# Performance work log

Measured on AMD Instinct MI355X. Metric: run time of the kernel, lower is better.

Reference implementation:

```python
import math
import jax, jax.numpy as jnp
import numpy as np

N, E = 40000, 640000
IN, OUT, T, R, H = 128, 128, 8, 16, 8
DK = OUT // H


def _tproj(x, W, types):
    # x: (N, I), W: (T, I, O), types: (N,) -> per-node type-indexed projection (N, O)
    allp = jnp.einsum('ni,tio->nto', x, W)  # T is tiny (8), cheap vs gathering per-node W
    return jnp.take_along_axis(allp, types[:, None, None], axis=1)[:, 0]


def setup_inputs() -> dict:
    key = jax.random.key(0)
    ks = jax.random.split(key, 12)
    h = jax.random.normal(ks[0], (N, IN), jnp.float32)
    src = jax.random.randint(ks[1], (E,), 0, N)
    dst = jax.random.randint(ks[2], (E,), 0, N)
    ntype = jax.random.randint(ks[3], (N,), 0, T)
    etype = jax.random.randint(ks[4], (E,), 0, R)
    s = 0.05  # scale torch.rand-style U(0,1) params for stable softmax numerics
    k_weight = jax.random.uniform(ks[5], (T, IN, OUT), jnp.float32) * s
    q_weight = jax.random.uniform(ks[6], (T, IN, OUT), jnp.float32) * s
    v_weight = jax.random.uniform(ks[7], (T, IN, OUT), jnp.float32) * s
    a_weight = jax.random.uniform(ks[8], (T, OUT, OUT), jnp.float32) * s
    relation_att = jax.random.uniform(ks[9], (R, H, DK, DK), jnp.float32) * s
    relation_msg = jax.random.uniform(ks[10], (R, H, DK, DK), jnp.float32) * s
    relation_pri = jnp.ones((R, H), jnp.float32)
    skip = jnp.ones((T, H), jnp.float32)
    return dict(h=h, k_weight=k_weight, q_weight=q_weight, v_weight=v_weight,
                a_weight=a_weight, relation_pri=relation_pri, relation_att=relation_att,
                relation_msg=relation_msg, skip=skip, src=src, dst=dst,
                ntype=ntype, etype=etype)


def reference(h, k_weight, q_weight, v_weight, a_weight, relation_pri,
              relation_att, relation_msg, skip, src, dst, ntype, etype):
    n, _ = h.shape
    nT, _, out = k_weight.shape
    nR, nH, dk, _ = relation_att.shape
    e = src.shape[0]
    sqrt_dk = math.sqrt(out)  # matches self.sqrt_dk = sqrt(out_feat_dim)

    # per-node type-specific k/v/q projections (equivalent to per-edge gathered bmm)
    k_n = _tproj(h, k_weight, ntype)
    v_n = _tproj(h, v_weight, ntype)
    q_n = _tproj(h, q_weight, ntype)

    k = k_n[src].reshape(e, nH, dk)
    v = v_n[src].reshape(e, nH, dk)
    q = q_n[dst].reshape(e, nH, dk)

    # relation-specific transforms; loop over small fixed relation set to avoid
    # materializing the (E, H, dk, dk) gathered weight tensor
    k2 = jnp.zeros_like(k)
    v2 = jnp.zeros_like(v)
    for r in range(nR):
        m = (etype == r)[:, None, None]
        k2 = k2 + jnp.where(m, jnp.einsum('ehd,hdc->ehc', k, relation_att[r]), 0.0)
        v2 = v2 + jnp.where(m, jnp.einsum('ehd,hdc->ehc', v, relation_msg[r]), 0.0)

    # attention score per edge/head
    attn = jnp.einsum('ehd,ehd->eh', k2, q) * relation_pri[etype] / sqrt_dk

    # segment (edge) softmax over destination nodes
    amax = jax.lax.stop_gradient(jax.ops.segment_max(attn, dst, num_segments=n))
    p = jnp.exp(attn - amax[dst])
    denom = jax.ops.segment_sum(p, dst, num_segments=n)
    alpha = p / denom[dst]  # (E, H)

    # weighted message scatter-sum -> mailbox reduce
    msg = alpha[:, :, None] * v2  # (E, H, dk)
    t = jax.ops.segment_sum(msg.reshape(e, nH * dk), dst, num_segments=n)  # (N, OUT)

    # node update: type-indexed output transform, per-head sigmoid skip gate
    trans = _tproj(t, a_weight, ntype)  # (N, OUT)
    gate = jax.nn.sigmoid(skip[ntype])  # (N, H)
    out_h = (trans.reshape(n, nH, dk) * gate[:, :, None]).reshape(n, out)
    return out_h


if __name__ == '__main__':
    inp = setup_inputs()
    o = reference(**inp)
    print(o.shape, o.dtype)
```

## Files before the change

### kernel.cpp

```cpp
#include <hip/hip_runtime.h>
#include <hip/hip_fp16.h>
#include <type_traits>

#define NN 40000
#define EE 640000
#define TT 8
#define RR 16
#define HH 8
#define DIM 128
#define NEG_BIG (-3.402823466e38f)
#define INV_SQRT_OUT 0.08838834764831845f


__global__ void zero_k(int* __restrict__ p, int n) {
  int i = blockIdx.x * blockDim.x + threadIdx.x;
  if (i < n) p[i] = 0;
}


__global__ void hist_nodes_k(const int* __restrict__ ntype, int* __restrict__ cnt_t) {
  __shared__ int lc[TT];
  int tid = threadIdx.x;
  if (tid < TT) lc[tid] = 0;
  __syncthreads();
  int n = blockIdx.x * blockDim.x + tid;
  if (n < NN) atomicAdd(&lc[ntype[n]], 1);
  __syncthreads();
  if (tid < TT && lc[tid]) atomicAdd(&cnt_t[tid], lc[tid]);
}

__global__ void hist_edges_k(const int* __restrict__ dst, const int* __restrict__ etype,
                             int* __restrict__ deg, int* __restrict__ cnt_r) {
  __shared__ int lc[RR];
  int tid = threadIdx.x;
  if (tid < RR) lc[tid] = 0;
  __syncthreads();
  int e = blockIdx.x * blockDim.x + tid;
  if (e < EE) {
    atomicAdd(&deg[dst[e]], 1);
    atomicAdd(&lc[etype[e]], 1);
  }
  __syncthreads();
  if (tid < RR && lc[tid]) atomicAdd(&cnt_r[tid], lc[tid]);
}

__global__ __launch_bounds__(1024) void scan_k(
    const int* __restrict__ cnt_t, int* __restrict__ toff, int* __restrict__ tcur,
    const int* __restrict__ cnt_r, int* __restrict__ roff, int* __restrict__ rcur,
    const int* __restrict__ deg, int* __restrict__ off, int* __restrict__ cur) {
  __shared__ int tot[1024];
  int tid = threadIdx.x;
  if (tid == 0) {
    int a = 0;
    for (int t = 0; t < TT; ++t) { toff[t] = a; tcur[t] = a; a += cnt_t[t]; }
    toff[TT] = a;
    a = 0;
    for (int r = 0; r < RR; ++r) { roff[r] = a; rcur[r] = a; a += cnt_r[r]; }
    roff[RR] = a;
  }
  const int NPT = (NN + 1023) / 1024;
  int base = tid * NPT;
  int s = 0;
  for (int k = 0; k < NPT; ++k) { int i = base + k; if (i < NN) s += deg[i]; }
  tot[tid] = s;
  __syncthreads();
  for (int st = 1; st < 1024; st <<= 1) {
    int v = (tid >= st) ? tot[tid - st] : 0;
    __syncthreads();
    tot[tid] += v;
    __syncthreads();
  }
  int run = (tid > 0) ? tot[tid - 1] : 0;
  for (int k = 0; k < NPT; ++k) {
    int i = base + k;
    if (i < NN) {
      cur[i] = run;
      run += deg[i];
      off[i + 1] = run;
    }
  }
  if (tid == 0) off[0] = 0;
}

__global__ void scatter_nodes_k(const int* __restrict__ ntype, int* __restrict__ tcur,
                                int* __restrict__ perm) {
  __shared__ int lc[TT], lb[TT];
  int tid = threadIdx.x;
  if (tid < TT) lc[tid] = 0;
  __syncthreads();
  int n = blockIdx.x * blockDim.x + tid;
  int t = 0, rank = 0;
  bool valid = (n < NN);
  if (valid) { t = ntype[n]; rank = atomicAdd(&lc[t], 1); }
  __syncthreads();
  if (tid < TT && lc[tid]) lb[tid] = atomicAdd(&tcur[tid], lc[tid]);
  __syncthreads();
  if (valid) perm[lb[t] + rank] = n;
}

__global__ void scatter_edges_k(const int* __restrict__ dst, const int* __restrict__ etype,
                                int* __restrict__ cur, int* __restrict__ rcur,
                                int* __restrict__ eid_dst, int* __restrict__ eid_r) {
  __shared__ int lc[RR], lb[RR];
  int tid = threadIdx.x;
  if (tid < RR) lc[tid] = 0;
  __syncthreads();
  int e = blockIdx.x * blockDim.x + tid;
  int r = 0, rank = 0;
  bool valid = (e < EE);
  if (valid) {
    int dd = dst[e];
    int p = atomicAdd(&cur[dd], 1);
    eid_dst[p] = e;
    r = etype[e];
    rank = atomicAdd(&lc[r], 1);
  }
  __syncthreads();
  if (tid < RR && lc[tid]) lb[tid] = atomicAdd(&rcur[tid], lc[tid]);
  __syncthreads();
  if (valid) eid_r[lb[r] + rank] = e;
}


template <int NMAT, bool GATE>
__global__ __launch_bounds__(256) void proj_k(
    const float* __restrict__ X,
    const float* __restrict__ W0, const float* __restrict__ W1, const float* __restrict__ W2,
    float* O0, float* O1, float* O2,
    const int* __restrict__ perm, const int* __restrict__ toff,
    const float* __restrict__ skipw) {
  __shared__ float xs[64 * DIM];
  __shared__ int pid[64];
  int t = blockIdx.y;
  int b0 = toff[t] + blockIdx.x * 64;
  int bn = toff[t + 1] - b0;
  if (bn <= 0) return;
  if (bn > 64) bn = 64;
  int tid = threadIdx.x;
  if (tid < 64) pid[tid] = perm[b0 + ((tid < bn) ? tid : 0)];
  __syncthreads();
  for (int s = tid; s < 64 * 32; s += 256) {
    int row = s >> 5, c4 = s & 31;
    *(float4*)&xs[row * DIM + c4 * 4] = *(const float4*)&X[(size_t)pid[row] * DIM + c4 * 4];
  }
  __syncthreads();
  int p = tid & 63, q = tid >> 6;
  int oc = 2 * p;
  float gate = 1.f;
  if (GATE) {
    float sk = skipw[t * HH + (oc >> 4)];
    gate = 1.f / (1.f + __expf(-sk));
  }
  const float* Ws[3] = {W0, W1, W2};
  float* Os[3] = {O0, O1, O2};
#pragma unroll
  for (int mat = 0; mat < NMAT; ++mat) {
    const float* W = Ws[mat] + (size_t)t * DIM * DIM;
    float acc0[16], acc1[16];
#pragma unroll
    for (int m = 0; m < 16; ++m) { acc0[m] = 0.f; acc1[m] = 0.f; }
    for (int i4 = 0; i4 < 32; ++i4) {
      int i = i4 * 4;
      float2 w0 = *(const float2*)&W[(i + 0) * DIM + oc];
      float2 w1 = *(const float2*)&W[(i + 1) * DIM + oc];
      float2 w2 = *(const float2*)&W[(i + 2) * DIM + oc];
      float2 w3 = *(const float2*)&W[(i + 3) * DIM + oc];
#pragma unroll
      for (int m = 0; m < 16; ++m) {
        float4 xv = *(const float4*)&xs[(q * 16 + m) * DIM + i];
        acc0[m] += xv.x * w0.x + xv.y * w1.x + xv.z * w2.x + xv.w * w3.x;
        acc1[m] += xv.x * w0.y + xv.y * w1.y + xv.z * w2.y + xv.w * w3.y;
      }
    }
    float* O = Os[mat];
#pragma unroll
    for (int m = 0; m < 16; ++m) {
      float2 val = {acc0[m] * gate, acc1[m] * gate};
      *(float2*)&O[(size_t)pid[q * 16 + m] * DIM + oc] = val;
    }
  }
}


template <typename VT, bool WV2>
__global__ __launch_bounds__(256) void edge_k(
    const float* __restrict__ kn, const float* __restrict__ qn, const float* __restrict__ vn,
    const float* __restrict__ attw, const float* __restrict__ msgw, const float* __restrict__ pri,
    const int* __restrict__ src, const int* __restrict__ dst,
    const int* __restrict__ roff, const int* __restrict__ eidr,
    float* __restrict__ attn_ws, VT* __restrict__ v2) {
  int r = blockIdx.y;
  int base = roff[r];
  int cnt = roff[r + 1] - base;
  int tile0 = blockIdx.x * 256;
  if (tile0 >= cnt) return;
  __shared__ float att_sw[2048];
  __shared__ float msg_sw[2048];
  __shared__ int eid[256];
  int tid = threadIdx.x;
  {
    const float* A = attw + (size_t)r * 2048;
    const float* M = msgw + (size_t)r * 2048;
    for (int idx = tid; idx < 2048; idx += 256) {
      int hh = idx >> 8, dd = (idx >> 4) & 15, cc = idx & 15;
      int u = ((((hh << 6) + (cc << 2) + (dd >> 2)) ^ hh) << 2) + (dd & 3);
      att_sw[u] = A[idx];
      if (WV2) msg_sw[u] = M[idx];
    }
  }
  eid[tid] = (tile0 + tid < cnt) ? eidr[base + tile0 + tid] : -1;
  __syncthreads();
  int h = tid & 7;
  float prih = pri[r * HH + h] * INV_SQRT_OUT;
  for (int pass = 0; pass < 8; ++pass) {
    int e = eid[(pass << 5) + (tid >> 3)];
    if (e < 0) continue;
    int s = src[e], d = dst[e];
    float kk[16], qq[16];
    const float* kp = kn + (size_t)s * DIM + h * 16;
    *(float4*)&kk[0] = *(const float4*)(kp + 0);
    *(float4*)&kk[4] = *(const float4*)(kp + 4);
    *(float4*)&kk[8] = *(const float4*)(kp + 8);
    *(float4*)&kk[12] = *(const float4*)(kp + 12);
    const float* qp = qn + (size_t)d * DIM + h * 16;
    *(float4*)&qq[0] = *(const float4*)(qp + 0);
    *(float4*)&qq[4] = *(const float4*)(qp + 4);
    *(float4*)&qq[8] = *(const float4*)(qp + 8);
    *(float4*)&qq[12] = *(const float4*)(qp + 12);
    float attn = 0.f;
#pragma unroll
    for (int c = 0; c < 16; ++c) {
      float k2c = 0.f;
#pragma unroll
      for (int dq = 0; dq < 4; ++dq) {
        float4 av = *(const float4*)&att_sw[((((h << 6) + (c << 2) + dq) ^ h) << 2)];
        k2c += kk[dq * 4 + 0] * av.x + kk[dq * 4 + 1] * av.y + kk[dq * 4 + 2] * av.z + kk[dq * 4 + 3] * av.w;
      }
      attn += k2c * qq[c];
    }
    attn_ws[(size_t)e * HH + h] = attn * prih;
    if constexpr (WV2) {
      float vv[16], o16[16];
      const float* vp = vn + (size_t)s * DIM + h * 16;
      *(float4*)&vv[0] = *(const float4*)(vp + 0);
      *(float4*)&vv[4] = *(const float4*)(vp + 4);
      *(float4*)&vv[8] = *(const float4*)(vp + 8);
      *(float4*)&vv[12] = *(const float4*)(vp + 12);
#pragma unroll
      for (int c = 0; c < 16; ++c) {
        float vc = 0.f;
#pragma unroll
        for (int dq = 0; dq < 4; ++dq) {
          float4 mv = *(const float4*)&msg_sw[((((h << 6) + (c << 2) + dq) ^ h) << 2)];
          vc += vv[dq * 4 + 0] * mv.x + vv[dq * 4 + 1] * mv.y + vv[dq * 4 + 2] * mv.z + vv[dq * 4 + 3] * mv.w;
        }
        o16[c] = vc;
      }
      VT* vo = v2 + (size_t)e * DIM + h * 16;
      if constexpr (std::is_same<VT, float>::value) {
        *(float4*)(vo + 0) = make_float4(o16[0], o16[1], o16[2], o16[3]);
        *(float4*)(vo + 4) = make_float4(o16[4], o16[5], o16[6], o16[7]);
        *(float4*)(vo + 8) = make_float4(o16[8], o16[9], o16[10], o16[11]);
        *(float4*)(vo + 12) = make_float4(o16[12], o16[13], o16[14], o16[15]);
      } else {
        __half2* vo2 = (__half2*)vo;
#pragma unroll
        for (int i = 0; i < 8; ++i) vo2[i] = __floats2half2_rn(o16[2 * i], o16[2 * i + 1]);
      }
    }
  }
}


__device__ __forceinline__ float ldv2(const float* p) { return *p; }
__device__ __forceinline__ float ldv2(const __half* p) { return __half2float(*p); }

__device__ __forceinline__ void softmax_stats(
    const int* __restrict__ eid_dst, const float* __restrict__ attn_ws,
    int beg, int end, int lane, float& MA, float& rA, float& MB, float& rB) {
  int j = lane >> 3, hh = lane & 7;
  float m = NEG_BIG, ssum = 0.f;
  for (int b = beg + j; b < end; b += 8) {
    int e = eid_dst[b];
    float a = attn_ws[(size_t)e * HH + hh];
    if (a > m) { ssum = ssum * __expf(m - a) + 1.f; m = a; }
    else ssum += __expf(a - m);
  }
#pragma unroll
  for (int mk = 8; mk <= 32; mk <<= 1) {
    float mo = __shfl_xor(m, mk);
    float so = __shfl_xor(ssum, mk);
    float M = fmaxf(m, mo);
    ssum = ssum * __expf(m - M) + so * __expf(mo - M);
    m = M;
  }
  int hA = lane >> 4, hB = hA + 4;
  MA = __shfl(m, hA);
  float SA = __shfl(ssum, hA);
  MB = __shfl(m, hB);
  float SB = __shfl(ssum, hB);
  rA = 1.f / SA;
  rB = 1.f / SB;
}

template <typename VT>
__global__ __launch_bounds__(256) void node_k(
    const int* __restrict__ off, const int* __restrict__ eid_dst,
    const float* __restrict__ attn_ws, const VT* __restrict__ v2,
    float* __restrict__ tbuf) {
  int wid = threadIdx.x >> 6, lane = threadIdx.x & 63;
  int n = blockIdx.x * 4 + wid;
  if (n >= NN) return;
  int beg = off[n], end = off[n + 1];
  float t0 = 0.f, t1 = 0.f;
  if (end > beg) {
    float MA, rA, MB, rB;
    softmax_stats(eid_dst, attn_ws, beg, end, lane, MA, rA, MB, rB);
    int hA = lane >> 4, hB = hA + 4;
    for (int b = beg; b < end; ++b) {
      int e = eid_dst[b];
      float aA = attn_ws[(size_t)e * HH + hA];
      float aB = attn_ws[(size_t)e * HH + hB];
      float wA = __expf(aA - MA) * rA;
      float wB = __expf(aB - MB) * rB;
      t0 += wA * ldv2(&v2[(size_t)e * DIM + lane]);
      t1 += wB * ldv2(&v2[(size_t)e * DIM + 64 + lane]);
    }
  }
  tbuf[(size_t)n * DIM + lane] = t0;
  tbuf[(size_t)n * DIM + 64 + lane] = t1;
}

__global__ __launch_bounds__(256) void node_rec_k(
    const int* __restrict__ off, const int* __restrict__ eid_dst,
    const float* __restrict__ attn_ws, const float* __restrict__ vn,
    const int* __restrict__ src, const int* __restrict__ etype,
    const float* __restrict__ msgw, float* __restrict__ tbuf) {
  int wid = threadIdx.x >> 6, lane = threadIdx.x & 63;
  int n = blockIdx.x * 4 + wid;
  if (n >= NN) return;
  int beg = off[n], end = off[n + 1];
  float t0 = 0.f, t1 = 0.f;
  if (end > beg) {
    float MA, rA, MB, rB;
    softmax_stats(eid_dst, attn_ws, beg, end, lane, MA, rA, MB, rB);
    int hA = lane >> 4, hB = hA + 4, c = lane & 15;
    for (int b = beg; b < end; ++b) {
      int e = eid_dst[b];
      int s = src[e], r = etype[e];
      float wA = __expf(attn_ws[(size_t)e * HH + hA] - MA) * rA;
      float wB = __expf(attn_ws[(size_t)e * HH + hB] - MB) * rB;
      const float* vpA = vn + (size_t)s * DIM + hA * 16;
      const float* vpB = vn + (size_t)s * DIM + hB * 16;
      const float* mpA = msgw + (size_t)r * 2048 + hA * 256 + c;
      const float* mpB = msgw + (size_t)r * 2048 + hB * 256 + c;
      float v2A = 0.f, v2B = 0.f;
#pragma unroll
      for (int d = 0; d < 16; ++d) {
        v2A += vpA[d] * mpA[d * 16];
        v2B += vpB[d] * mpB[d * 16];
      }
      t0 += wA * v2A;
      t1 += wB * v2B;
    }
  }
  tbuf[(size_t)n * DIM + lane] = t0;
  tbuf[(size_t)n * DIM + 64 + lane] = t1;
}


extern "C" void kernel_launch(void* const* d_in, const int* in_sizes, int n_in,
                              void* d_out, int out_size, void* d_ws, size_t ws_size,
                              hipStream_t stream) {
  const float* h_in = (const float*)d_in[0];
  const float* k_w = (const float*)d_in[1];
  const float* q_w = (const float*)d_in[2];
  const float* v_w = (const float*)d_in[3];
  const float* a_w = (const float*)d_in[4];
  const float* pri = (const float*)d_in[5];
  const float* att = (const float*)d_in[6];
  const float* msgw = (const float*)d_in[7];
  const float* skipw = (const float*)d_in[8];
  const int* src = (const int*)d_in[9];
  const int* dst = (const int*)d_in[10];
  const int* ntype = (const int*)d_in[11];
  const int* etype = (const int*)d_in[12];
  float* out = (float*)d_out;

  char* w = (char*)d_ws;
  size_t o = 0;
  auto take = [&](size_t bytes) -> char* {
    char* p = w + o;
    o += (bytes + 255) & ~(size_t)255;
    return p;
  };
  float* kn = (float*)take((size_t)NN * DIM * 4);
  float* qn = (float*)take((size_t)NN * DIM * 4);
  float* vn = (float*)take((size_t)NN * DIM * 4);
  float* attn_ws = (float*)take((size_t)EE * HH * 4);
  int* small = (int*)take(1024);
  int* deg = (int*)take((size_t)NN * 4);
  int* off = (int*)take((size_t)(NN + 1) * 4);
  int* cur = (int*)take((size_t)(NN + 1) * 4);
  int* perm = (int*)take((size_t)NN * 4);
  int* eidd = (int*)take((size_t)EE * 4);
  int* eidr = (int*)take((size_t)EE * 4);
  size_t fixed_end = o;
  float* tb = kn;

  int* cnt_t = small;
  int* toff = small + 8;
  int* tcur = small + 17;
  int* cnt_r = small + 25;
  int* roff = small + 41;
  int* rcur = small + 58;

  zero_k<<<(256 + NN + 255) / 256, 256, 0, stream>>>(small, 256 + NN);

  hist_nodes_k<<<(NN + 255) / 256, 256, 0, stream>>>(ntype, cnt_t);
  hist_edges_k<<<(EE + 255) / 256, 256, 0, stream>>>(dst, etype, deg, cnt_r);
  scan_k<<<1, 1024, 0, stream>>>(cnt_t, toff, tcur, cnt_r, roff, rcur, deg, off, cur);
  scatter_nodes_k<<<(NN + 255) / 256, 256, 0, stream>>>(ntype, tcur, perm);
  scatter_edges_k<<<(EE + 255) / 256, 256, 0, stream>>>(dst, etype, cur, rcur, eidd, eidr);

  proj_k<3, false><<<dim3(112, TT), 256, 0, stream>>>(h_in, k_w, q_w, v_w, kn, qn, vn, perm, toff, nullptr);

  size_t need32 = fixed_end + (size_t)EE * DIM * 4;
  size_t need16 = fixed_end + (size_t)EE * DIM * 2;
  if (ws_size >= need32) {
    float* v2 = (float*)(w + fixed_end);
    edge_k<float, true><<<dim3(176, RR), 256, 0, stream>>>(kn, qn, vn, att, msgw, pri, src, dst, roff, eidr, attn_ws, v2);
    node_k<float><<<(NN + 3) / 4, 256, 0, stream>>>(off, eidd, attn_ws, v2, tb);
  } else if (ws_size >= need16) {
    __half* v2 = (__half*)(w + fixed_end);
    edge_k<__half, true><<<dim3(176, RR), 256, 0, stream>>>(kn, qn, vn, att, msgw, pri, src, dst, roff, eidr, attn_ws, v2);
    node_k<__half><<<(NN + 3) / 4, 256, 0, stream>>>(off, eidd, attn_ws, v2, tb);
  } else {
    edge_k<float, false><<<dim3(176, RR), 256, 0, stream>>>(kn, qn, vn, att, msgw, pri, src, dst, roff, eidr, attn_ws, (float*)nullptr);
    node_rec_k<<<(NN + 3) / 4, 256, 0, stream>>>(off, eidd, attn_ws, vn, src, etype, msgw, tb);
  }

  proj_k<1, true><<<dim3(112, TT), 256, 0, stream>>>(tb, a_w, a_w, a_w, out, out, out, perm, toff, skipw);
}
```

Baseline: 679.0 us.

## Write edge outputs in dst-sorted order and pack src/dst indices

```diff
diff --git a/kernel.cpp b/kernel.cpp
--- a/kernel.cpp
+++ b/kernel.cpp
@@ -17,6 +17,25 @@
   if (i < n) p[i] = 0;
 }
 
+__device__ __forceinline__ void load16f(const float* p, float* o) {
+  *(float4*)&o[0]  = *(const float4*)(p + 0);
+  *(float4*)&o[4]  = *(const float4*)(p + 4);
+  *(float4*)&o[8]  = *(const float4*)(p + 8);
+  *(float4*)&o[12] = *(const float4*)(p + 12);
+}
+
+__device__ __forceinline__ float dot16(const float* a, const float* c) {
+  float s0 = fmaf(a[0], c[0], a[1] * c[1]);
+  float s1 = fmaf(a[2], c[2], a[3] * c[3]);
+  float s2 = fmaf(a[4], c[4], a[5] * c[5]);
+  float s3 = fmaf(a[6], c[6], a[7] * c[7]);
+  s0 = fmaf(a[8], c[8], s0);  s1 = fmaf(a[9], c[9], s1);
+  s2 = fmaf(a[10], c[10], s2); s3 = fmaf(a[11], c[11], s3);
+  s0 = fmaf(a[12], c[12], s0); s1 = fmaf(a[13], c[13], s1);
+  s2 = fmaf(a[14], c[14], s2); s3 = fmaf(a[15], c[15], s3);
+  return (s0 + s1) + (s2 + s3);
+}
+
 
 __global__ void hist_nodes_k(const int* __restrict__ ntype, int* __restrict__ cnt_t) {
   __shared__ int lc[TT];
@@ -98,27 +117,45 @@
   if (valid) perm[lb[t] + rank] = n;
 }
 
-__global__ void scatter_edges_k(const int* __restrict__ dst, const int* __restrict__ etype,
+__global__ void scatter_edges_k(const int* __restrict__ src, const int* __restrict__ dst,
+                                const int* __restrict__ etype,
                                 int* __restrict__ cur, int* __restrict__ rcur,
-                                int* __restrict__ eid_dst, int* __restrict__ eid_r) {
+                                int* __restrict__ epack, int* __restrict__ epos) {
   __shared__ int lc[RR], lb[RR];
   int tid = threadIdx.x;
   if (tid < RR) lc[tid] = 0;
   __syncthreads();
   int e = blockIdx.x * blockDim.x + tid;
-  int r = 0, rank = 0;
+  int r = 0, rank = 0, p = 0;
+  unsigned int pk = 0;
   bool valid = (e < EE);
   if (valid) {
-    int dd = dst[e];
-    int p = atomicAdd(&cur[dd], 1);
-    eid_dst[p] = e;
+    int sv = src[e], dv = dst[e];
+    p = atomicAdd(&cur[dv], 1);
+    pk = ((unsigned int)sv << 16) | (unsigned int)dv;
     r = etype[e];
     rank = atomicAdd(&lc[r], 1);
   }
   __syncthreads();
   if (tid < RR && lc[tid]) lb[tid] = atomicAdd(&rcur[tid], lc[tid]);
   __syncthreads();
-  if (valid) eid_r[lb[r] + rank] = e;
+  if (valid) {
+    int j = lb[r] + rank;
+    epack[j] = (int)pk;
+    epos[j] = p;
+  }
+}
+
+
+__global__ void prep_k(const float* __restrict__ attw, const float* __restrict__ msgw,
+                       const float* __restrict__ pri,
+                       float* __restrict__ attT, float* __restrict__ msgT) {
+  int i = blockIdx.x * 256 + threadIdx.x;
+  if (i >= RR * HH * 256) return;
+  int d = i & 15, c = (i >> 4) & 15, rh = i >> 8;
+  float scale = pri[rh] * INV_SQRT_OUT;
+  attT[i] = attw[(rh << 8) + (d << 4) + c] * scale;
+  msgT[i] = msgw[(rh << 8) + (d << 4) + c];
 }
 
 
@@ -182,190 +219,116 @@
 }
 
 
-template <typename VT, bool WV2>
-__global__ __launch_bounds__(256) void edge_k(
+__global__ __launch_bounds__(256) void edge2_k(
     const float* __restrict__ kn, const float* __restrict__ qn, const float* __restrict__ vn,
-    const float* __restrict__ attw, const float* __restrict__ msgw, const float* __restrict__ pri,
-    const int* __restrict__ src, const int* __restrict__ dst,
-    const int* __restrict__ roff, const int* __restrict__ eidr,
-    float* __restrict__ attn_ws, VT* __restrict__ v2) {
+    const float* __restrict__ attT, const float* __restrict__ msgT,
+    const int* __restrict__ epack, const int* __restrict__ epos, const int* __restrict__ roff,
+    float* __restrict__ attn_ws, __half* __restrict__ v2) {
   int r = blockIdx.y;
-  int base = roff[r];
-  int cnt = roff[r + 1] - base;
-  int tile0 = blockIdx.x * 256;
-  if (tile0 >= cnt) return;
-  __shared__ float att_sw[2048];
-  __shared__ float msg_sw[2048];
-  __shared__ int eid[256];
-  int tid = threadIdx.x;
-  {
-    const float* A = attw + (size_t)r * 2048;
-    const float* M = msgw + (size_t)r * 2048;
-    for (int idx = tid; idx < 2048; idx += 256) {
-      int hh = idx >> 8, dd = (idx >> 4) & 15, cc = idx & 15;
-      int u = ((((hh << 6) + (cc << 2) + (dd >> 2)) ^ hh) << 2) + (dd & 3);
-      att_sw[u] = A[idx];
-      if (WV2) msg_sw[u] = M[idx];
-    }
-  }
-  eid[tid] = (tile0 + tid < cnt) ? eidr[base + tile0 + tid] : -1;
-  __syncthreads();
-  int h = tid & 7;
-  float prih = pri[r * HH + h] * INV_SQRT_OUT;
-  for (int pass = 0; pass < 8; ++pass) {
-    int e = eid[(pass << 5) + (tid >> 3)];
-    if (e < 0) continue;
-    int s = src[e], d = dst[e];
-    float kk[16], qq[16];
-    const float* kp = kn + (size_t)s * DIM + h * 16;
-    *(float4*)&kk[0] = *(const float4*)(kp + 0);
-    *(float4*)&kk[4] = *(const float4*)(kp + 4);
-    *(float4*)&kk[8] = *(const float4*)(kp + 8);
-    *(float4*)&kk[12] = *(const float4*)(kp + 12);
-    const float* qp = qn + (size_t)d * DIM + h * 16;
-    *(float4*)&qq[0] = *(const float4*)(qp + 0);
-    *(float4*)&qq[4] = *(const float4*)(qp + 4);
-    *(float4*)&qq[8] = *(const float4*)(qp + 8);
-    *(float4*)&qq[12] = *(const float4*)(qp + 12);
-    float attn = 0.f;
+  int base = roff[r], cnt = roff[r + 1] - base;
+  int t0 = blockIdx.x * 512;
+  if (t0 >= cnt) return;
+  int tid = threadIdx.x;
+  int i0 = t0 + tid, i1 = i0 + 256;
+  bool e0v = i0 < cnt, e1v = i1 < cnt;
+  unsigned int ep0 = e0v ? (unsigned int)epack[base + i0] : 0u;
+  unsigned int ep1 = e1v ? (unsigned int)epack[base + i1] : 0u;
+  int p0 = e0v ? epos[base + i0] : 0;
+  int p1 = e1v ? epos[base + i1] : 0;
+  int s0 = ep0 >> 16, d0 = ep0 & 0xffff;
+  int s1 = ep1 >> 16, d1 = ep1 & 0xffff;
+  const float* aT = attT + (r << 11);
+  const float* mT = msgT + (r << 11);
+#pragma unroll 1
+  for (int h = 0; h < 8; ++h) {
+    float ka[16], kb[16], qa[16], qb[16];
+    load16f(kn + (s0 << 7) + (h << 4), ka);
+    load16f(kn + (s1 << 7) + (h << 4), kb);
+    load16f(qn + (d0 << 7) + (h << 4), qa);
+    load16f(qn + (d1 << 7) + (h << 4), qb);
+    float at0 = 0.f, at1 = 0.f;
 #pragma unroll
     for (int c = 0; c < 16; ++c) {
-      float k2c = 0.f;
-#pragma unroll
-      for (int dq = 0; dq < 4; ++dq) {
-        float4 av = *(const float4*)&att_sw[((((h << 6) + (c << 2) + dq) ^ h) << 2)];
-        k2c += kk[dq * 4 + 0] * av.x + kk[dq * 4 + 1] * av.y + kk[dq * 4 + 2] * av.z + kk[dq * 4 + 3] * av.w;
-      }
-      attn += k2c * qq[c];
-    }
-    attn_ws[(size_t)e * HH + h] = attn * prih;
-    if constexpr (WV2) {
-      float vv[16], o16[16];
-      const float* vp = vn + (size_t)s * DIM + h * 16;
-      *(float4*)&vv[0] = *(const float4*)(vp + 0);
-      *(float4*)&vv[4] = *(const float4*)(vp + 4);
-      *(float4*)&vv[8] = *(const float4*)(vp + 8);
-      *(float4*)&vv[12] = *(const float4*)(vp + 12);
-#pragma unroll
-      for (int c = 0; c < 16; ++c) {
-        float vc = 0.f;
-#pragma unroll
-        for (int dq = 0; dq < 4; ++dq) {
-          float4 mv = *(const float4*)&msg_sw[((((h << 6) + (c << 2) + dq) ^ h) << 2)];
-          vc += vv[dq * 4 + 0] * mv.x + vv[dq * 4 + 1] * mv.y + vv[dq * 4 + 2] * mv.z + vv[dq * 4 + 3] * mv.w;
-        }
-        o16[c] = vc;
-      }
-      VT* vo = v2 + (size_t)e * DIM + h * 16;
-      if constexpr (std::is_same<VT, float>::value) {
-        *(float4*)(vo + 0) = make_float4(o16[0], o16[1], o16[2], o16[3]);
-        *(float4*)(vo + 4) = make_float4(o16[4], o16[5], o16[6], o16[7]);
-        *(float4*)(vo + 8) = make_float4(o16[8], o16[9], o16[10], o16[11]);
-        *(float4*)(vo + 12) = make_float4(o16[12], o16[13], o16[14], o16[15]);
-      } else {
-        __half2* vo2 = (__half2*)vo;
-#pragma unroll
-        for (int i = 0; i < 8; ++i) vo2[i] = __floats2half2_rn(o16[2 * i], o16[2 * i + 1]);
-      }
-    }
-  }
-}
-
-
-__device__ __forceinline__ float ldv2(const float* p) { return *p; }
-__device__ __forceinline__ float ldv2(const __half* p) { return __half2float(*p); }
-
-__device__ __forceinline__ void softmax_stats(
-    const int* __restrict__ eid_dst, const float* __restrict__ attn_ws,
-    int beg, int end, int lane, float& MA, float& rA, float& MB, float& rB) {
-  int j = lane >> 3, hh = lane & 7;
-  float m = NEG_BIG, ssum = 0.f;
-  for (int b = beg + j; b < end; b += 8) {
-    int e = eid_dst[b];
-    float a = attn_ws[(size_t)e * HH + hh];
-    if (a > m) { ssum = ssum * __expf(m - a) + 1.f; m = a; }
-    else ssum += __expf(a - m);
-  }
-#pragma unroll
-  for (int mk = 8; mk <= 32; mk <<= 1) {
-    float mo = __shfl_xor(m, mk);
-    float so = __shfl_xor(ssum, mk);
-    float M = fmaxf(m, mo);
-    ssum = ssum * __expf(m - M) + so * __expf(mo - M);
-    m = M;
-  }
-  int hA = lane >> 4, hB = hA + 4;
-  MA = __shfl(m, hA);
-  float SA = __shfl(ssum, hA);
-  MB = __shfl(m, hB);
-  float SB = __shfl(ssum, hB);
-  rA = 1.f / SA;
-  rB = 1.f / SB;
-}
-
-template <typename VT>
-__global__ __launch_bounds__(256) void node_k(
-    const int* __restrict__ off, const int* __restrict__ eid_dst,
-    const float* __restrict__ attn_ws, const VT* __restrict__ v2,
-    float* __restrict__ tbuf) {
+      const float* col = aT + (h << 8) + (c << 4);
+      float k20 = dot16(ka, col);
+      float k21 = dot16(kb, col);
+      at0 = fmaf(k20, qa[c], at0);
+      at1 = fmaf(k21, qb[c], at1);
+    }
+    if (e0v) attn_ws[(p0 << 3) + h] = at0;
+    if (e1v) attn_ws[(p1 << 3) + h] = at1;
+    float va[16], vb[16];
+    load16f(vn + (s0 << 7) + (h << 4), va);
+    load16f(vn + (s1 << 7) + (h << 4), vb);
+    float o0[16], o1[16];
+#pragma unroll
+    for (int c = 0; c < 16; ++c) {
+      const float* col = mT + (h << 8) + (c << 4);
+      o0[c] = dot16(va, col);
+      o1[c] = dot16(vb, col);
+    }
+    if (e0v) {
+      unsigned int wd[8];
+      union { unsigned int v; __half2 h2; } cv;
+#pragma unroll
+      for (int i = 0; i < 8; ++i) { cv.h2 = __floats2half2_rn(o0[2 * i], o0[2 * i + 1]); wd[i] = cv.v; }
+      uint4* dst4 = (uint4*)(v2 + (p0 << 7) + (h << 4));
+      dst4[0] = make_uint4(wd[0], wd[1], wd[2], wd[3]);
+      dst4[1] = make_uint4(wd[4], wd[5], wd[6], wd[7]);
+    }
+    if (e1v) {
+      unsigned int wd[8];
+      union { unsigned int v; __half2 h2; } cv;
+#pragma unroll
+      for (int i = 0; i < 8; ++i) { cv.h2 = __floats2half2_rn(o1[2 * i], o1[2 * i + 1]); wd[i] = cv.v; }
+      uint4* dst4 = (uint4*)(v2 + (p1 << 7) + (h << 4));
+      dst4[0] = make_uint4(wd[0], wd[1], wd[2], wd[3]);
+      dst4[1] = make_uint4(wd[4], wd[5], wd[6], wd[7]);
+    }
+  }
+}
+
+
+__global__ __launch_bounds__(256) void node2_k(
+    const int* __restrict__ off, const float* __restrict__ attn_ws,
+    const __half* __restrict__ v2, float* __restrict__ tbuf) {
   int wid = threadIdx.x >> 6, lane = threadIdx.x & 63;
   int n = blockIdx.x * 4 + wid;
   if (n >= NN) return;
   int beg = off[n], end = off[n + 1];
-  float t0 = 0.f, t1 = 0.f;
+  float tx = 0.f, ty = 0.f;
   if (end > beg) {
-    float MA, rA, MB, rB;
-    softmax_stats(eid_dst, attn_ws, beg, end, lane, MA, rA, MB, rB);
-    int hA = lane >> 4, hB = hA + 4;
+    int j = lane >> 3, h = lane & 7;
+    float m = NEG_BIG, ss = 0.f;
+    for (int b = beg + j; b < end; b += 8) {
+      float a = attn_ws[(b << 3) + h];
+      if (a > m) { ss = ss * __expf(m - a) + 1.f; m = a; }
+      else ss += __expf(a - m);
+    }
+#pragma unroll
+    for (int mk = 8; mk <= 32; mk <<= 1) {
+      float mo = __shfl_xor(m, mk);
+      float so = __shfl_xor(ss, mk);
+      float M = fmaxf(m, mo);
+      ss = ss * __expf(m - M) + so * __expf(mo - M);
+      m = M;
+    }
+    int hh = lane >> 3;
+    float M = __shfl(m, hh);
+    float R = 1.f / __shfl(ss, hh);
+    const unsigned int* vp = (const unsigned int*)v2;
     for (int b = beg; b < end; ++b) {
-      int e = eid_dst[b];
-      float aA = attn_ws[(size_t)e * HH + hA];
-      float aB = attn_ws[(size_t)e * HH + hB];
-      float wA = __expf(aA - MA) * rA;
-      float wB = __expf(aB - MB) * rB;
-      t0 += wA * ldv2(&v2[(size_t)e * DIM + lane]);
-      t1 += wB * ldv2(&v2[(size_t)e * DIM + 64 + lane]);
-    }
-  }
-  tbuf[(size_t)n * DIM + lane] = t0;
-  tbuf[(size_t)n * DIM + 64 + lane] = t1;
-}
-
-__global__ __launch_bounds__(256) void node_rec_k(
-    const int* __restrict__ off, const int* __restrict__ eid_dst,
-    const float* __restrict__ attn_ws, const float* __restrict__ vn,
-    const int* __restrict__ src, const int* __restrict__ etype,
-    const float* __restrict__ msgw, float* __restrict__ tbuf) {
-  int wid = threadIdx.x >> 6, lane = threadIdx.x & 63;
-  int n = blockIdx.x * 4 + wid;
-  if (n >= NN) return;
-  int beg = off[n], end = off[n + 1];
-  float t0 = 0.f, t1 = 0.f;
-  if (end > beg) {
-    float MA, rA, MB, rB;
-    softmax_stats(eid_dst, attn_ws, beg, end, lane, MA, rA, MB, rB);
-    int hA = lane >> 4, hB = hA + 4, c = lane & 15;
-    for (int b = beg; b < end; ++b) {
-      int e = eid_dst[b];
-      int s = src[e], r = etype[e];
-      float wA = __expf(attn_ws[(size_t)e * HH + hA] - MA) * rA;
-      float wB = __expf(attn_ws[(size_t)e * HH + hB] - MB) * rB;
-      const float* vpA = vn + (size_t)s * DIM + hA * 16;
-      const float* vpB = vn + (size_t)s * DIM + hB * 16;
-      const float* mpA = msgw + (size_t)r * 2048 + hA * 256 + c;
-      const float* mpB = msgw + (size_t)r * 2048 + hB * 256 + c;
-      float v2A = 0.f, v2B = 0.f;
-#pragma unroll
-      for (int d = 0; d < 16; ++d) {
-        v2A += vpA[d] * mpA[d * 16];
-        v2B += vpB[d] * mpB[d * 16];
-      }
-      t0 += wA * v2A;
-      t1 += wB * v2B;
-    }
-  }
-  tbuf[(size_t)n * DIM + lane] = t0;
-  tbuf[(size_t)n * DIM + 64 + lane] = t1;
+      float a = attn_ws[(b << 3) + hh];
+      float w = __expf(a - M) * R;
+      union { unsigned int v; __half2 h2; } cv;
+      cv.v = vp[(b << 6) + lane];
+      float2 f = __half22float2(cv.h2);
+      tx = fmaf(w, f.x, tx);
+      ty = fmaf(w, f.y, ty);
+    }
+  }
+  float2 t = {tx, ty};
+  *(float2*)&tbuf[((size_t)n << 7) + (lane << 1)] = t;
 }
 
 
@@ -398,14 +361,16 @@
   float* qn = (float*)take((size_t)NN * DIM * 4);
   float* vn = (float*)take((size_t)NN * DIM * 4);
   float* attn_ws = (float*)take((size_t)EE * HH * 4);
+  float* attT = (float*)take((size_t)RR * HH * 256 * 4);
+  float* msgT = (float*)take((size_t)RR * HH * 256 * 4);
   int* small = (int*)take(1024);
   int* deg = (int*)take((size_t)NN * 4);
   int* off = (int*)take((size_t)(NN + 1) * 4);
   int* cur = (int*)take((size_t)(NN + 1) * 4);
   int* perm = (int*)take((size_t)NN * 4);
-  int* eidd = (int*)take((size_t)EE * 4);
-  int* eidr = (int*)take((size_t)EE * 4);
-  size_t fixed_end = o;
+  int* epack = (int*)take((size_t)EE * 4);
+  int* epos = (int*)take((size_t)EE * 4);
+  __half* v2 = (__half*)take((size_t)EE * DIM * 2);
   float* tb = kn;
 
   int* cnt_t = small;
@@ -421,24 +386,16 @@
   hist_edges_k<<<(EE + 255) / 256, 256, 0, stream>>>(dst, etype, deg, cnt_r);
   scan_k<<<1, 1024, 0, stream>>>(cnt_t, toff, tcur, cnt_r, roff, rcur, deg, off, cur);
   scatter_nodes_k<<<(NN + 255) / 256, 256, 0, stream>>>(ntype, tcur, perm);
-  scatter_edges_k<<<(EE + 255) / 256, 256, 0, stream>>>(dst, etype, cur, rcur, eidd, eidr);
-
-  proj_k<3, false><<<dim3(112, TT), 256, 0, stream>>>(h_in, k_w, q_w, v_w, kn, qn, vn, perm, toff, nullptr);
-
-  size_t need32 = fixed_end + (size_t)EE * DIM * 4;
-  size_t need16 = fixed_end + (size_t)EE * DIM * 2;
-  if (ws_size >= need32) {
-    float* v2 = (float*)(w + fixed_end);
-    edge_k<float, true><<<dim3(176, RR), 256, 0, stream>>>(kn, qn, vn, att, msgw, pri, src, dst, roff, eidr, attn_ws, v2);
-    node_k<float><<<(NN + 3) / 4, 256, 0, stream>>>(off, eidd, attn_ws, v2, tb);
-  } else if (ws_size >= need16) {
-    __half* v2 = (__half*)(w + fixed_end);
-    edge_k<__half, true><<<dim3(176, RR), 256, 0, stream>>>(kn, qn, vn, att, msgw, pri, src, dst, roff, eidr, attn_ws, v2);
-    node_k<__half><<<(NN + 3) / 4, 256, 0, stream>>>(off, eidd, attn_ws, v2, tb);
-  } else {
-    edge_k<float, false><<<dim3(176, RR), 256, 0, stream>>>(kn, qn, vn, att, msgw, pri, src, dst, roff, eidr, attn_ws, (float*)nullptr);
-    node_rec_k<<<(NN + 3) / 4, 256, 0, stream>>>(off, eidd, attn_ws, vn, src, etype, msgw, tb);
-  }
-
-  proj_k<1, true><<<dim3(112, TT), 256, 0, stream>>>(tb, a_w, a_w, a_w, out, out, out, perm, toff, skipw);
-}
+  scatter_edges_k<<<(EE + 255) / 256, 256, 0, stream>>>(src, dst, etype, cur, rcur, epack, epos);
+  prep_k<<<(RR * HH * 256 + 255) / 256, 256, 0, stream>>>(att, msgw, pri, attT, msgT);
+
+  proj_k<3, false><<<dim3(112, TT), 256, 0, stream>>>(
+      h_in, k_w, q_w, v_w, kn, qn, vn, perm, toff, nullptr);
+
+  edge2_k<<<dim3(88, RR), 256, 0, stream>>>(kn, qn, vn, attT, msgT, epack, epos, roff, attn_ws, v2);
+
+  node2_k<<<(NN + 3) / 4, 256, 0, stream>>>(off, attn_ws, v2, tb);
+
+  proj_k<1, true><<<dim3(112, TT), 256, 0, stream>>>(
+      tb, a_w, a_w, a_w, out, out, out, perm, toff, skipw);
+}
```

Result: slower. 885.2 us (+30.4%).
